# Kernel optimization log

Hardware: AMD Instinct MI355X
Metric: run time of the kernel (lower is better)

The kernel has to match this reference:

```python
import jax, jax.numpy as jnp
import numpy as np

VOCAB = 50257
HID = 1024
MAXLEN = 64


def setup_inputs() -> dict:
    key = jax.random.key(0)
    ks = jax.random.split(key, 12)
    s = 1.0 / np.sqrt(HID)
    return {
        "input": jax.random.randint(ks[0], (1,), 0, VOCAB),
        "hidden": jax.random.normal(ks[1], (1, 1, HID), jnp.float32),
        "enc_outputs": jax.random.normal(ks[2], (MAXLEN, HID), jnp.float32),
        "emb": jax.random.normal(ks[3], (VOCAB, HID), jnp.float32),
        "attn_W": jax.random.uniform(ks[4], (MAXLEN, 2 * HID), jnp.float32, -s, s),
        "attn_b": jnp.zeros((MAXLEN,), jnp.float32),
        "comb_W": jax.random.uniform(ks[5], (HID, 2 * HID), jnp.float32, -s, s),
        "comb_b": jnp.zeros((HID,), jnp.float32),
        "gru_Wih": jax.random.uniform(ks[6], (3 * HID, HID), jnp.float32, -s, s),
        "gru_Whh": jax.random.uniform(ks[7], (3 * HID, HID), jnp.float32, -s, s),
        "gru_bih": jnp.zeros((3 * HID,), jnp.float32),
        "gru_bhh": jnp.zeros((3 * HID,), jnp.float32),
        "out_W": jax.random.uniform(ks[8], (VOCAB, HID), jnp.float32, -s, s),
        "out_b": jnp.zeros((VOCAB,), jnp.float32),
    }


def reference(input, hidden, enc_outputs, emb, attn_W, attn_b, comb_W, comb_b,
              gru_Wih, gru_Whh, gru_bih, gru_bhh, out_W, out_b):
    # embedded: [1, HID] (dropout is identity in eval / p=0)
    embedded = emb[input[0]][None, :]
    h = hidden[0]  # [1, HID]
    # attention over encoder positions
    cat_eh = jnp.concatenate([embedded, h], axis=1)           # [1, 2H]
    attn_weights = jax.nn.softmax(cat_eh @ attn_W.T + attn_b, axis=1)  # [1, MAXLEN]
    attn_applied = attn_weights @ enc_outputs                  # [1, HID]
    # combine
    x = jnp.concatenate([embedded, attn_applied], axis=1)      # [1, 2H]
    x = jax.nn.relu(x @ comb_W.T + comb_b)                     # [1, HID]
    # single GRU step (PyTorch gate order: r, z, n)
    gi = x @ gru_Wih.T + gru_bih                                # [1, 3H]
    gh = h @ gru_Whh.T + gru_bhh                                # [1, 3H]
    i_r, i_z, i_n = jnp.split(gi, 3, axis=1)
    h_r, h_z, h_n = jnp.split(gh, 3, axis=1)
    r = jax.nn.sigmoid(i_r + h_r)
    z = jax.nn.sigmoid(i_z + h_z)
    n = jnp.tanh(i_n + r * h_n)
    h_new = (1.0 - z) * n + z * h                               # [1, HID]
    # output projection + log-softmax
    logp = jax.nn.log_softmax(h_new @ out_W.T + out_b, axis=1)  # [1, VOCAB]
    return logp, h_new[None, :, :], attn_weights
```

## Files before the change

kernel.cpp:

```cpp
#include <hip/hip_runtime.h>
#include <hip/hip_bf16.h>

#define VOCAB 50257
#define HID   1024
#define MAXLEN 64

__device__ __forceinline__ float dot4(float4 a, float4 b){
  return a.x*b.x + a.y*b.y + a.z*b.z + a.w*b.w;
}
__device__ __forceinline__ float dot4f(float4 a, const float* v){
  return a.x*v[0] + a.y*v[1] + a.z*v[2] + a.w*v[3];
}

__global__ __launch_bounds__(256) void k_attn_scores(
    const int* tok_p, const float* hidden, const float* emb,
    const float* attn_W, const float* attn_b, float* ws_scores){
  int b = blockIdx.x, t = threadIdx.x;
  int tok = min(max(tok_p[0], 0), VOCAB-1);
  const float4* wv = (const float4*)(attn_W + (size_t)b*2048);
  const float4* ef = (const float4*)(emb + (size_t)tok*HID);
  const float4* hf = (const float4*)hidden;
  float acc = dot4(wv[t], ef[t]) + dot4(wv[256+t], hf[t]);
  #pragma unroll
  for (int k=32;k>=1;k>>=1) acc += __shfl_xor(acc,k);
  __shared__ float red[4];
  if ((t&63)==0) red[t>>6] = acc;
  __syncthreads();
  if (t==0) ws_scores[b] = red[0]+red[1]+red[2]+red[3] + attn_b[b];
}

__global__ __launch_bounds__(1024) void k_softmax_attn(
    const float* ws_scores, const float* enc,
    float* ws_attn, float* out_attn){
  int t = threadIdx.x;
  __shared__ float sw[MAXLEN];
  if (t < 64) {
    float s = ws_scores[t];
    float m = s;
    #pragma unroll
    for (int k=32;k>=1;k>>=1) m = fmaxf(m, __shfl_xor(m,k));
    float e = expf(s-m), d = e;
    #pragma unroll
    for (int k=32;k>=1;k>>=1) d += __shfl_xor(d,k);
    float w = e/d;
    sw[t] = w;
    out_attn[t] = w;
  }
  __syncthreads();
  float acc = 0.f;
  #pragma unroll 8
  for (int p=0;p<MAXLEN;p++) acc += sw[p]*enc[p*HID + t];
  ws_attn[t] = acc;
}

__global__ __launch_bounds__(256) void k_combine(
    const int* tok_p, const float* ws_attn, const float* emb,
    const float* comb_W, const float* comb_b, float* ws_x){
  int wave = threadIdx.x>>6, lane = threadIdx.x&63;
  int row = blockIdx.x*4 + wave;
  int tok = min(max(tok_p[0], 0), VOCAB-1);
  const float4* wrow = (const float4*)(comb_W + (size_t)row*2048);
  const float4* erow = (const float4*)(emb + (size_t)tok*HID);
  const float4* av   = (const float4*)ws_attn;
  float acc = 0.f;
  #pragma unroll
  for (int c=0;c<4;c++) acc += dot4(wrow[c*64+lane],     erow[c*64+lane]);
  #pragma unroll
  for (int c=0;c<4;c++) acc += dot4(wrow[256+c*64+lane], av[c*64+lane]);
  #pragma unroll
  for (int k=32;k>=1;k>>=1) acc += __shfl_xor(acc,k);
  if (lane==0) ws_x[row] = fmaxf(acc + comb_b[row], 0.f);
}

__global__ __launch_bounds__(256) void k_gru_mv(
    const float* ws_x, const float* hidden,
    const float* Wih, const float* Whh,
    const float* bih, const float* bhh,
    float* ws_gi, float* ws_gh){
  int wave = threadIdx.x>>6, lane = threadIdx.x&63;
  int g = blockIdx.x*4 + wave;
  bool ih = g < 3*HID;
  int row = ih ? g : g - 3*HID;
  const float* W = ih ? Wih : Whh;
  const float4* wrow = (const float4*)(W + (size_t)row*HID);
  const float4* vec  = ih ? (const float4*)ws_x : (const float4*)hidden;
  float acc = 0.f;
  #pragma unroll
  for (int c=0;c<4;c++) acc += dot4(wrow[c*64+lane], vec[c*64+lane]);
  #pragma unroll
  for (int k=32;k>=1;k>>=1) acc += __shfl_xor(acc,k);
  if (lane==0) {
    if (ih) ws_gi[row] = acc + bih[row];
    else    ws_gh[row] = acc + bhh[row];
  }
}

__global__ __launch_bounds__(1024) void k_gru_gate(
    const float* gi, const float* gh, const float* hidden,
    float* ws_h, float* out_h){
  int t = threadIdx.x;
  float r = 1.f/(1.f+expf(-(gi[t]        + gh[t])));
  float z = 1.f/(1.f+expf(-(gi[HID+t]    + gh[HID+t])));
  float n = tanhf(gi[2*HID+t] + r*gh[2*HID+t]);
  float h = hidden[t];
  float hn = (1.f-z)*n + z*h;
  ws_h[t] = hn;
  out_h[t] = hn;
}

__global__ __launch_bounds__(256) void k_logits(
    const float* wsh, const float* out_W, const float* out_b,
    float* out_logits, float* ws_stats){
  int wave = threadIdx.x>>6, lane = threadIdx.x&63;
  int gw = blockIdx.x*4 + wave;
  float hv[16];
  #pragma unroll
  for (int c=0;c<4;c++)
    #pragma unroll
    for (int j=0;j<4;j++) hv[c*4+j] = wsh[c*256 + lane*4 + j];
  float m = -INFINITY, s = 0.f;
  for (int row = gw; row < VOCAB; row += 8192) {
    const float4* wrow = (const float4*)(out_W + (size_t)row*HID);
    float acc = 0.f;
    #pragma unroll
    for (int c=0;c<4;c++) acc += dot4f(wrow[c*64+lane], hv + c*4);
    #pragma unroll
    for (int k=32;k>=1;k>>=1) acc += __shfl_xor(acc,k);
    if (lane==0) {
      float logit = acc + out_b[row];
      out_logits[row] = logit;
      if (logit > m) { s = s*expf(m-logit) + 1.f; m = logit; }
      else s += expf(logit-m);
    }
  }
  __shared__ float sm[4], ss[4];
  if (lane==0){ sm[wave]=m; ss[wave]=s; }
  __syncthreads();
  if (threadIdx.x==0) {
    float M = fmaxf(fmaxf(sm[0],sm[1]),fmaxf(sm[2],sm[3]));
    float S = ss[0]*expf(sm[0]-M)+ss[1]*expf(sm[1]-M)
            + ss[2]*expf(sm[2]-M)+ss[3]*expf(sm[3]-M);
    ws_stats[blockIdx.x*2]   = M;
    ws_stats[blockIdx.x*2+1] = S;
  }
}

__global__ __launch_bounds__(256) void k_lse(const float* ws_stats, float* ws_lse){
  int t = threadIdx.x;
  float m = -INFINITY, s = 0.f;
  for (int i=t;i<2048;i+=256){
    float mi = ws_stats[2*i], si = ws_stats[2*i+1];
    float M = fmaxf(m,mi);
    s = s*expf(m-M) + si*expf(mi-M);
    m = M;
  }
  #pragma unroll
  for (int k=32;k>=1;k>>=1){
    float mo = __shfl_xor(m,k), so = __shfl_xor(s,k);
    float M = fmaxf(m,mo);
    s = s*expf(m-M) + so*expf(mo-M);
    m = M;
  }
  __shared__ float sm[4], ss[4];
  if ((t&63)==0){ sm[t>>6]=m; ss[t>>6]=s; }
  __syncthreads();
  if (t==0){
    float M = fmaxf(fmaxf(sm[0],sm[1]),fmaxf(sm[2],sm[3]));
    float S = ss[0]*expf(sm[0]-M)+ss[1]*expf(sm[1]-M)
            + ss[2]*expf(sm[2]-M)+ss[3]*expf(sm[3]-M);
    ws_lse[0] = M + logf(S);
  }
}

__global__ __launch_bounds__(256) void k_logp(float* out_logits, const float* ws_lse){
  int i = blockIdx.x*256 + threadIdx.x;
  if (i < VOCAB) out_logits[i] = out_logits[i] - ws_lse[0];
}

extern "C" void kernel_launch(void* const* d_in, const int* in_sizes, int n_in,
                              void* d_out, int out_size, void* d_ws, size_t ws_size,
                              hipStream_t stream) {
  const int*   tok    = (const int*)d_in[0];
  const float* hidden = (const float*)d_in[1];
  const float* enc    = (const float*)d_in[2];
  const float* emb    = (const float*)d_in[3];
  const float* attn_W = (const float*)d_in[4];
  const float* attn_b = (const float*)d_in[5];
  const float* comb_W = (const float*)d_in[6];
  const float* comb_b = (const float*)d_in[7];
  const float* Wih    = (const float*)d_in[8];
  const float* Whh    = (const float*)d_in[9];
  const float* bih    = (const float*)d_in[10];
  const float* bhh    = (const float*)d_in[11];
  const float* out_W  = (const float*)d_in[12];
  const float* out_b  = (const float*)d_in[13];

  float* out      = (float*)d_out;
  float* out_logp = out;
  float* out_h    = out + VOCAB;
  float* out_attn = out + VOCAB + HID;

  float* ws        = (float*)d_ws;
  float* ws_scores = ws;
  float* ws_attn   = ws + 128;
  float* ws_x      = ws + 1152;
  float* ws_gi     = ws + 2176;
  float* ws_gh     = ws + 5248;
  float* ws_h      = ws + 8320;
  float* ws_stats  = ws + 9344;
  float* ws_lse    = ws + 13440;

  k_attn_scores <<<64,   256, 0, stream>>>(tok, hidden, emb, attn_W, attn_b, ws_scores);
  k_softmax_attn<<<1,    1024,0, stream>>>(ws_scores, enc, ws_attn, out_attn);
  k_combine     <<<256,  256, 0, stream>>>(tok, ws_attn, emb, comb_W, comb_b, ws_x);
  k_gru_mv      <<<1536, 256, 0, stream>>>(ws_x, hidden, Wih, Whh, bih, bhh, ws_gi, ws_gh);
  k_gru_gate    <<<1,    1024,0, stream>>>(ws_gi, ws_gh, hidden, ws_h, out_h);
  k_logits      <<<2048, 256, 0, stream>>>(ws_h, out_W, out_b, out_logp, ws_stats);
  k_lse         <<<1,    256, 0, stream>>>(ws_stats, ws_lse);
  k_logp        <<<197,  256, 0, stream>>>(out_logp, ws_lse);
}
```

Baseline: 423.1 us.

## Fuse decoder stages into two persistent kernels with grid-wide atomic barriers

Replaces eight small launches with an init kernel plus two persistent-grid kernels. The stages run in those kernels separated by atomic-counter grid barriers, which removes per-launch overhead and idle gaps between dependent stages. The Whh matvec now runs alongside the attention scores. The logits kernel keeps logits in registers, reduces the log-sum-exp after a grid barrier and writes log-probs once, so the separate lse and logp passes and the extra read-modify-write of the logits go away. The barriers assume all 1024 blocks are co-resident, which risks deadlock if occupancy falls short.

```diff
diff --git a/kernel.cpp b/kernel.cpp
--- a/kernel.cpp
+++ b/kernel.cpp
@@ -4,6 +4,8 @@
 #define VOCAB 50257
 #define HID   1024
 #define MAXLEN 64
+#define G_PRE 1024
+#define G_LOG 1024
 
 __device__ __forceinline__ float dot4(float4 a, float4 b){
   return a.x*b.x + a.y*b.y + a.z*b.z + a.w*b.w;
@@ -11,170 +13,207 @@
 __device__ __forceinline__ float dot4f(float4 a, const float* v){
   return a.x*v[0] + a.y*v[1] + a.z*v[2] + a.w*v[3];
 }
-
-__global__ __launch_bounds__(256) void k_attn_scores(
-    const int* tok_p, const float* hidden, const float* emb,
-    const float* attn_W, const float* attn_b, float* ws_scores){
-  int b = blockIdx.x, t = threadIdx.x;
+__device__ __forceinline__ float wave_sum(float acc){
+  #pragma unroll
+  for (int k=32;k>=1;k>>=1) acc += __shfl_xor(acc,k);
+  return acc;
+}
+
+__device__ __forceinline__ void gbar(unsigned* cnt, unsigned target){
+  __syncthreads();
+  if (threadIdx.x==0){
+    __hip_atomic_fetch_add(cnt, 1u, __ATOMIC_RELEASE, __HIP_MEMORY_SCOPE_AGENT);
+    while (__hip_atomic_load(cnt, __ATOMIC_ACQUIRE, __HIP_MEMORY_SCOPE_AGENT) < target)
+      __builtin_amdgcn_s_sleep(8);
+  }
+  __syncthreads();
+}
+
+__global__ __launch_bounds__(64) void k_init(unsigned* bar){
+  if (threadIdx.x < 16) bar[threadIdx.x] = 0u;
+}
+
+__global__ __launch_bounds__(256,4) void k_pre(
+    const int* tok_p, const float* hidden, const float* enc, const float* emb,
+    const float* attn_W, const float* attn_b,
+    const float* comb_W, const float* comb_b,
+    const float* Wih, const float* Whh, const float* bih, const float* bhh,
+    float* out_h, float* out_attn, unsigned* bar, float* ws)
+{
+  float* ws_scores = ws + 64;
+  float* ws_attn   = ws + 128;
+  float* ws_x      = ws + 1280;
+  float* ws_gi     = ws + 2304;
+  float* ws_gh     = ws + 5376;
+  float* ws_h      = ws + 8448;
+
+  int t = threadIdx.x, lane = t&63;
+  int gw = blockIdx.x*4 + (t>>6);
   int tok = min(max(tok_p[0], 0), VOCAB-1);
-  const float4* wv = (const float4*)(attn_W + (size_t)b*2048);
-  const float4* ef = (const float4*)(emb + (size_t)tok*HID);
-  const float4* hf = (const float4*)hidden;
-  float acc = dot4(wv[t], ef[t]) + dot4(wv[256+t], hf[t]);
-  #pragma unroll
-  for (int k=32;k>=1;k>>=1) acc += __shfl_xor(acc,k);
-  __shared__ float red[4];
-  if ((t&63)==0) red[t>>6] = acc;
-  __syncthreads();
-  if (t==0) ws_scores[b] = red[0]+red[1]+red[2]+red[3] + attn_b[b];
-}
-
-__global__ __launch_bounds__(1024) void k_softmax_attn(
-    const float* ws_scores, const float* enc,
-    float* ws_attn, float* out_attn){
-  int t = threadIdx.x;
   __shared__ float sw[MAXLEN];
-  if (t < 64) {
-    float s = ws_scores[t];
-    float m = s;
-    #pragma unroll
-    for (int k=32;k>=1;k>>=1) m = fmaxf(m, __shfl_xor(m,k));
-    float e = expf(s-m), d = e;
-    #pragma unroll
-    for (int k=32;k>=1;k>>=1) d += __shfl_xor(d,k);
-    float w = e/d;
-    sw[t] = w;
-    out_attn[t] = w;
-  }
-  __syncthreads();
-  float acc = 0.f;
-  #pragma unroll 8
-  for (int p=0;p<MAXLEN;p++) acc += sw[p]*enc[p*HID + t];
-  ws_attn[t] = acc;
-}
-
-__global__ __launch_bounds__(256) void k_combine(
-    const int* tok_p, const float* ws_attn, const float* emb,
-    const float* comb_W, const float* comb_b, float* ws_x){
-  int wave = threadIdx.x>>6, lane = threadIdx.x&63;
-  int row = blockIdx.x*4 + wave;
-  int tok = min(max(tok_p[0], 0), VOCAB-1);
-  const float4* wrow = (const float4*)(comb_W + (size_t)row*2048);
-  const float4* erow = (const float4*)(emb + (size_t)tok*HID);
-  const float4* av   = (const float4*)ws_attn;
-  float acc = 0.f;
-  #pragma unroll
-  for (int c=0;c<4;c++) acc += dot4(wrow[c*64+lane],     erow[c*64+lane]);
-  #pragma unroll
-  for (int c=0;c<4;c++) acc += dot4(wrow[256+c*64+lane], av[c*64+lane]);
-  #pragma unroll
-  for (int k=32;k>=1;k>>=1) acc += __shfl_xor(acc,k);
-  if (lane==0) ws_x[row] = fmaxf(acc + comb_b[row], 0.f);
-}
-
-__global__ __launch_bounds__(256) void k_gru_mv(
-    const float* ws_x, const float* hidden,
-    const float* Wih, const float* Whh,
-    const float* bih, const float* bhh,
-    float* ws_gi, float* ws_gh){
-  int wave = threadIdx.x>>6, lane = threadIdx.x&63;
-  int g = blockIdx.x*4 + wave;
-  bool ih = g < 3*HID;
-  int row = ih ? g : g - 3*HID;
-  const float* W = ih ? Wih : Whh;
-  const float4* wrow = (const float4*)(W + (size_t)row*HID);
-  const float4* vec  = ih ? (const float4*)ws_x : (const float4*)hidden;
-  float acc = 0.f;
-  #pragma unroll
-  for (int c=0;c<4;c++) acc += dot4(wrow[c*64+lane], vec[c*64+lane]);
-  #pragma unroll
-  for (int k=32;k>=1;k>>=1) acc += __shfl_xor(acc,k);
-  if (lane==0) {
-    if (ih) ws_gi[row] = acc + bih[row];
-    else    ws_gh[row] = acc + bhh[row];
-  }
-}
-
-__global__ __launch_bounds__(1024) void k_gru_gate(
-    const float* gi, const float* gh, const float* hidden,
-    float* ws_h, float* out_h){
-  int t = threadIdx.x;
-  float r = 1.f/(1.f+expf(-(gi[t]        + gh[t])));
-  float z = 1.f/(1.f+expf(-(gi[HID+t]    + gh[HID+t])));
-  float n = tanhf(gi[2*HID+t] + r*gh[2*HID+t]);
-  float h = hidden[t];
-  float hn = (1.f-z)*n + z*h;
-  ws_h[t] = hn;
-  out_h[t] = hn;
-}
-
-__global__ __launch_bounds__(256) void k_logits(
-    const float* wsh, const float* out_W, const float* out_b,
-    float* out_logits, float* ws_stats){
-  int wave = threadIdx.x>>6, lane = threadIdx.x&63;
-  int gw = blockIdx.x*4 + wave;
+
+  if (gw < 64) {
+    const float4* w4 = (const float4*)(attn_W + (size_t)gw*2048);
+    const float4* e4 = (const float4*)(emb + (size_t)tok*HID);
+    const float4* h4 = (const float4*)hidden;
+    float acc = 0.f;
+    #pragma unroll
+    for (int j=0;j<4;j++) acc += dot4(w4[j*64+lane], e4[j*64+lane]);
+    #pragma unroll
+    for (int j=0;j<4;j++) acc += dot4(w4[(j+4)*64+lane], h4[j*64+lane]);
+    acc = wave_sum(acc);
+    if (lane==0) ws_scores[gw] = acc + attn_b[gw];
+  } else if (gw >= 1024) {
+    int row = gw - 1024;
+    const float4* w4 = (const float4*)(Whh + (size_t)row*HID);
+    const float4* h4 = (const float4*)hidden;
+    float acc = 0.f;
+    #pragma unroll
+    for (int j=0;j<4;j++) acc += dot4(w4[j*64+lane], h4[j*64+lane]);
+    acc = wave_sum(acc);
+    if (lane==0) ws_gh[row] = acc + bhh[row];
+  }
+  gbar(bar+0, G_PRE);
+
+  if (blockIdx.x < 4) {
+    if (t < 64) {
+      float s = ws_scores[t];
+      float m = s;
+      #pragma unroll
+      for (int k=32;k>=1;k>>=1) m = fmaxf(m, __shfl_xor(m,k));
+      float e = expf(s-m);
+      float d = e;
+      #pragma unroll
+      for (int k=32;k>=1;k>>=1) d += __shfl_xor(d,k);
+      float w = e/d;
+      sw[t] = w;
+      if (blockIdx.x==0) out_attn[t] = w;
+    }
+    __syncthreads();
+    int idx = blockIdx.x*256 + t;
+    float acc = 0.f;
+    #pragma unroll 8
+    for (int p=0;p<MAXLEN;p++) acc += sw[p]*enc[p*HID + idx];
+    ws_attn[idx] = acc;
+  }
+  gbar(bar+1, G_PRE);
+
+  if (gw < 1024) {
+    const float4* w4 = (const float4*)(comb_W + (size_t)gw*2048);
+    const float4* e4 = (const float4*)(emb + (size_t)tok*HID);
+    const float4* a4 = (const float4*)ws_attn;
+    float acc = 0.f;
+    #pragma unroll
+    for (int j=0;j<4;j++) acc += dot4(w4[j*64+lane],     e4[j*64+lane]);
+    #pragma unroll
+    for (int j=0;j<4;j++) acc += dot4(w4[(j+4)*64+lane], a4[j*64+lane]);
+    acc = wave_sum(acc);
+    if (lane==0) ws_x[gw] = fmaxf(acc + comb_b[gw], 0.f);
+  }
+  gbar(bar+2, G_PRE);
+
+  if (gw < 3072) {
+    const float4* w4 = (const float4*)(Wih + (size_t)gw*HID);
+    const float4* x4 = (const float4*)ws_x;
+    float acc = 0.f;
+    #pragma unroll
+    for (int j=0;j<4;j++) acc += dot4(w4[j*64+lane], x4[j*64+lane]);
+    acc = wave_sum(acc);
+    if (lane==0) ws_gi[gw] = acc + bih[gw];
+  }
+  gbar(bar+3, G_PRE);
+
+  if (blockIdx.x < 4) {
+    int i = blockIdx.x*256 + t;
+    float r = 1.f/(1.f+expf(-(ws_gi[i]      + ws_gh[i])));
+    float z = 1.f/(1.f+expf(-(ws_gi[HID+i]  + ws_gh[HID+i])));
+    float n = tanhf(ws_gi[2*HID+i] + r*ws_gh[2*HID+i]);
+    float h = hidden[i];
+    float hn = (1.f-z)*n + z*h;
+    ws_h[i]  = hn;
+    out_h[i] = hn;
+  }
+}
+
+__global__ __launch_bounds__(256,4) void k_logits_full(
+    const float* out_W, const float* out_b,
+    float* out_logp, unsigned* bar, float* ws)
+{
+  float* ws_h     = ws + 8448;
+  float* ws_stats = ws + 9600;
+  int t = threadIdx.x, lane = t&63, wv = t>>6;
+  int gw = blockIdx.x*4 + wv;
+
   float hv[16];
-  #pragma unroll
-  for (int c=0;c<4;c++)
-    #pragma unroll
-    for (int j=0;j<4;j++) hv[c*4+j] = wsh[c*256 + lane*4 + j];
+  const float4* h4 = (const float4*)ws_h;
+  #pragma unroll
+  for (int c=0;c<4;c++){
+    float4 v = h4[c*64+lane];
+    hv[c*4+0]=v.x; hv[c*4+1]=v.y; hv[c*4+2]=v.z; hv[c*4+3]=v.w;
+  }
+
+  float lv[13];
   float m = -INFINITY, s = 0.f;
-  for (int row = gw; row < VOCAB; row += 8192) {
-    const float4* wrow = (const float4*)(out_W + (size_t)row*HID);
-    float acc = 0.f;
-    #pragma unroll
-    for (int c=0;c<4;c++) acc += dot4f(wrow[c*64+lane], hv + c*4);
-    #pragma unroll
-    for (int k=32;k>=1;k>>=1) acc += __shfl_xor(acc,k);
-    if (lane==0) {
-      float logit = acc + out_b[row];
-      out_logits[row] = logit;
-      if (logit > m) { s = s*expf(m-logit) + 1.f; m = logit; }
-      else s += expf(logit-m);
-    }
-  }
-  __shared__ float sm[4], ss[4];
-  if (lane==0){ sm[wave]=m; ss[wave]=s; }
-  __syncthreads();
-  if (threadIdx.x==0) {
+  int nr = 0;
+  #pragma unroll 1
+  for (int i=0;i<13;i++){
+    int row = gw + 4096*i;
+    if (row >= VOCAB) break;
+    const float4* w4 = (const float4*)(out_W + (size_t)row*HID);
+    float acc = 0.f;
+    #pragma unroll
+    for (int c=0;c<4;c++) acc += dot4f(w4[c*64+lane], hv + c*4);
+    acc = wave_sum(acc);
+    float logit = acc + out_b[row];
+    lv[i] = logit;
+    if (logit > m) { s = s*expf(m-logit) + 1.f; m = logit; }
+    else s += expf(logit-m);
+    nr++;
+  }
+
+  __shared__ float sm[4], ss[4], flse;
+  if (lane==0){ sm[wv]=m; ss[wv]=s; }
+  __syncthreads();
+  if (t==0){
     float M = fmaxf(fmaxf(sm[0],sm[1]),fmaxf(sm[2],sm[3]));
     float S = ss[0]*expf(sm[0]-M)+ss[1]*expf(sm[1]-M)
             + ss[2]*expf(sm[2]-M)+ss[3]*expf(sm[3]-M);
     ws_stats[blockIdx.x*2]   = M;
     ws_stats[blockIdx.x*2+1] = S;
   }
-}
-
-__global__ __launch_bounds__(256) void k_lse(const float* ws_stats, float* ws_lse){
-  int t = threadIdx.x;
-  float m = -INFINITY, s = 0.f;
-  for (int i=t;i<2048;i+=256){
-    float mi = ws_stats[2*i], si = ws_stats[2*i+1];
-    float M = fmaxf(m,mi);
-    s = s*expf(m-M) + si*expf(mi-M);
-    m = M;
+  gbar(bar+4, G_LOG);
+
+  float M = -INFINITY, S = 0.f;
+  #pragma unroll
+  for (int j=0;j<4;j++){
+    int b = t*4 + j;
+    float mi = ws_stats[b*2], si = ws_stats[b*2+1];
+    float Mn = fmaxf(M, mi);
+    S = S*expf(M-Mn) + si*expf(mi-Mn);
+    M = Mn;
   }
   #pragma unroll
   for (int k=32;k>=1;k>>=1){
-    float mo = __shfl_xor(m,k), so = __shfl_xor(s,k);
-    float M = fmaxf(m,mo);
-    s = s*expf(m-M) + so*expf(mo-M);
-    m = M;
-  }
-  __shared__ float sm[4], ss[4];
-  if ((t&63)==0){ sm[t>>6]=m; ss[t>>6]=s; }
+    float mo = __shfl_xor(M,k), so = __shfl_xor(S,k);
+    float Mn = fmaxf(M,mo);
+    S = S*expf(M-Mn) + so*expf(mo-Mn);
+    M = Mn;
+  }
+  if (lane==0){ sm[wv]=M; ss[wv]=S; }
   __syncthreads();
   if (t==0){
-    float M = fmaxf(fmaxf(sm[0],sm[1]),fmaxf(sm[2],sm[3]));
-    float S = ss[0]*expf(sm[0]-M)+ss[1]*expf(sm[1]-M)
-            + ss[2]*expf(sm[2]-M)+ss[3]*expf(sm[3]-M);
-    ws_lse[0] = M + logf(S);
-  }
-}
-
-__global__ __launch_bounds__(256) void k_logp(float* out_logits, const float* ws_lse){
-  int i = blockIdx.x*256 + threadIdx.x;
-  if (i < VOCAB) out_logits[i] = out_logits[i] - ws_lse[0];
+    float Mf = fmaxf(fmaxf(sm[0],sm[1]),fmaxf(sm[2],sm[3]));
+    float Sf = ss[0]*expf(sm[0]-Mf)+ss[1]*expf(sm[1]-Mf)
+             + ss[2]*expf(sm[2]-Mf)+ss[3]*expf(sm[3]-Mf);
+    flse = Mf + logf(Sf);
+  }
+  __syncthreads();
+  float lse = flse;
+
+  if (lane==0){
+    #pragma unroll 1
+    for (int i=0;i<nr;i++) out_logp[gw + 4096*i] = lv[i] - lse;
+  }
 }
 
 extern "C" void kernel_launch(void* const* d_in, const int* in_sizes, int n_in,
@@ -200,22 +239,12 @@
   float* out_h    = out + VOCAB;
   float* out_attn = out + VOCAB + HID;
 
-  float* ws        = (float*)d_ws;
-  float* ws_scores = ws;
-  float* ws_attn   = ws + 128;
-  float* ws_x      = ws + 1152;
-  float* ws_gi     = ws + 2176;
-  float* ws_gh     = ws + 5248;
-  float* ws_h      = ws + 8320;
-  float* ws_stats  = ws + 9344;
-  float* ws_lse    = ws + 13440;
-
-  k_attn_scores <<<64,   256, 0, stream>>>(tok, hidden, emb, attn_W, attn_b, ws_scores);
-  k_softmax_attn<<<1,    1024,0, stream>>>(ws_scores, enc, ws_attn, out_attn);
-  k_combine     <<<256,  256, 0, stream>>>(tok, ws_attn, emb, comb_W, comb_b, ws_x);
-  k_gru_mv      <<<1536, 256, 0, stream>>>(ws_x, hidden, Wih, Whh, bih, bhh, ws_gi, ws_gh);
-  k_gru_gate    <<<1,    1024,0, stream>>>(ws_gi, ws_gh, hidden, ws_h, out_h);
-  k_logits      <<<2048, 256, 0, stream>>>(ws_h, out_W, out_b, out_logp, ws_stats);
-  k_lse         <<<1,    256, 0, stream>>>(ws_stats, ws_lse);
-  k_logp        <<<197,  256, 0, stream>>>(out_logp, ws_lse);
-}
+  float*    ws  = (float*)d_ws;
+  unsigned* bar = (unsigned*)d_ws;
+
+  k_init<<<1, 64, 0, stream>>>(bar);
+  k_pre<<<G_PRE, 256, 0, stream>>>(tok, hidden, enc, emb, attn_W, attn_b,
+                                   comb_W, comb_b, Wih, Whh, bih, bhh,
+                                   out_h, out_attn, bar, ws);
+  k_logits_full<<<G_LOG, 256, 0, stream>>>(out_W, out_b, out_logp, bar, ws);
+}
```

New measurement: 958.2 us. 126% more time.
